# Kernel optimization log

Measured on AMD Instinct MI355X. Metric: run time of the kernel, lower is better.

## Reference

```python
import jax, jax.numpy as jnp
import numpy as np

B, S, HID = 2, 2048, 2048
NH, NKV, D = 16, 8, 128
EPS = 1e-6
THETA = 10000.0


def _rms_norm(x, w):
    # RMSNorm over last dim (head_dim), Qwen3-style per-head q/k norm
    var = jnp.mean(jnp.square(x), axis=-1, keepdims=True)
    return x * jax.lax.rsqrt(var + EPS) * w


def _rotate_half(x):
    x1, x2 = jnp.split(x, 2, axis=-1)
    return jnp.concatenate([-x2, x1], axis=-1)


def setup_inputs() -> dict:
    key = jax.random.key(0)
    ks = jax.random.split(key, 8)
    hidden_states = jax.random.normal(ks[0], (B, S, HID), dtype=jnp.float32)
    # rotary embeddings (HF-style: emb = concat(freqs, freqs))
    inv_freq = 1.0 / (THETA ** (jnp.arange(0, D, 2, dtype=jnp.float32) / D))
    pos = jnp.arange(S, dtype=jnp.float32)
    freqs = jnp.outer(pos, inv_freq)                      # [S, D/2]
    emb = jnp.concatenate([freqs, freqs], axis=-1)        # [S, D]
    cos = jnp.broadcast_to(jnp.cos(emb)[None], (B, S, D))
    sin = jnp.broadcast_to(jnp.sin(emb)[None], (B, S, D))
    w_scale = 1.0 / np.sqrt(HID)
    Wq = jax.random.normal(ks[1], (HID, NH * D), dtype=jnp.float32) * w_scale
    Wk = jax.random.normal(ks[2], (HID, NKV * D), dtype=jnp.float32) * w_scale
    Wv = jax.random.normal(ks[3], (HID, NKV * D), dtype=jnp.float32) * w_scale
    Wo = jax.random.normal(ks[4], (NH * D, HID), dtype=jnp.float32) * w_scale
    q_norm_w = jnp.ones((D,), dtype=jnp.float32)
    k_norm_w = jnp.ones((D,), dtype=jnp.float32)
    return {"hidden_states": hidden_states, "cos": cos, "sin": sin,
            "Wq": Wq, "Wk": Wk, "Wv": Wv, "Wo": Wo,
            "q_norm_w": q_norm_w, "k_norm_w": k_norm_w}


def reference(hidden_states, cos, sin, Wq, Wk, Wv, Wo, q_norm_w, k_norm_w):
    b, s, _ = hidden_states.shape
    # projections + per-head RMSNorm on q/k, then [B,H,S,D]
    q = _rms_norm((hidden_states @ Wq).reshape(b, s, NH, D), q_norm_w)
    k = _rms_norm((hidden_states @ Wk).reshape(b, s, NKV, D), k_norm_w)
    v = (hidden_states @ Wv).reshape(b, s, NKV, D)
    q = jnp.swapaxes(q, 1, 2)  # [B,NH,S,D]
    k = jnp.swapaxes(k, 1, 2)  # [B,NKV,S,D]
    v = jnp.swapaxes(v, 1, 2)
    # rotary position embedding
    c = cos[:, None, :, :]
    sn = sin[:, None, :, :]
    q = q * c + _rotate_half(q) * sn
    k = k * c + _rotate_half(k) * sn
    # GQA: expand kv heads to match query heads
    rep = NH // NKV
    k = jnp.repeat(k, rep, axis=1)
    v = jnp.repeat(v, rep, axis=1)
    # scaled causal attention (splash_attention semantics, causal mask)
    q = q * (D ** -0.5)
    scores = jnp.einsum('bhqd,bhkd->bhqk', q, k)
    causal = jnp.tril(jnp.ones((s, s), dtype=bool))
    scores = jnp.where(causal[None, None], scores, jnp.finfo(scores.dtype).min)
    attn = jax.nn.softmax(scores, axis=-1)
    out = jnp.einsum('bhqk,bhkd->bhqd', attn, v)
    out = jnp.swapaxes(out, 1, 2).reshape(b, s, NH * D)
    return out @ Wo
```

## Files before the change

### kernel.cpp

```cpp
#include <hip/hip_runtime.h>
#include <hip/hip_bf16.h>

typedef unsigned short u16;
typedef unsigned int u32;
typedef unsigned long long u64;
typedef __attribute__((ext_vector_type(8))) short short8;
typedef __attribute__((ext_vector_type(4))) float floatx4;

#define AS1 __attribute__((address_space(1)))
#define AS3 __attribute__((address_space(3)))

__device__ __forceinline__ float bf2f(u16 u) {
    u32 x = ((u32)u) << 16;
    float f;
    __builtin_memcpy(&f, &x, 4);
    return f;
}
__device__ __forceinline__ u16 f2bf(float f) {
    u32 x;
    __builtin_memcpy(&x, &f, 4);
    u32 r = (x + 0x7fffu + ((x >> 16) & 1u)) >> 16;
    return (u16)r;
}
__device__ __forceinline__ u32 f2bf_pk(float a, float b) {
    __hip_bfloat162 h = __float22bfloat162_rn(float2{a, b});
    u32 r;
    __builtin_memcpy(&r, &h, 4);
    return r;
}

__global__ __launch_bounds__(256) void convert_x(const float* __restrict__ in,
                                                 u16* __restrict__ out) {
    int i = blockIdx.x * 256 + threadIdx.x;
    float4 v = *(const float4*)(in + (size_t)i * 4);
    u16 o[4] = {f2bf(v.x), f2bf(v.y), f2bf(v.z), f2bf(v.w)};
    *(u64*)(out + (size_t)i * 4) = *(u64*)o;
}

__global__ __launch_bounds__(1024) void transpose_wall(const float* __restrict__ Wq,
                                                       const float* __restrict__ Wk,
                                                       const float* __restrict__ Wv,
                                                       const float* __restrict__ Wo,
                                                       u16* __restrict__ WqkvT,
                                                       u16* __restrict__ WoT) {
    const int z = blockIdx.z;
    const float* in;
    u16* out;
    int C;
    if (z == 0) { in = Wq; out = WqkvT; C = 2048; }
    else if (z == 1) { in = Wk; out = WqkvT + 2048 * 2048; C = 1024; }
    else if (z == 2) { in = Wv; out = WqkvT + 3072 * 2048; C = 1024; }
    else { in = Wo; out = WoT; C = 2048; }
    const int c0 = blockIdx.x * 32, r0 = blockIdx.y * 32;
    if (c0 >= C) return;
    __shared__ u16 t[32][33];
    const int tx = threadIdx.x, ty = threadIdx.y;
    t[ty][tx] = f2bf(in[(size_t)(r0 + ty) * C + c0 + tx]);
    __syncthreads();
    out[(size_t)(c0 + ty) * 2048 + r0 + tx] = t[tx][ty];
}

__global__ __launch_bounds__(1024) void transpose_v(const u16* __restrict__ QKV,
                                                    u16* __restrict__ Vt) {
    __shared__ u16 t[32][33];
    const int tx = threadIdx.x, ty = threadIdx.y;
    const int b = blockIdx.z >> 3, kv = blockIdx.z & 7;
    const int s0 = blockIdx.x * 32, d0 = blockIdx.y * 32;
    t[ty][tx] = QKV[(size_t)(b * 2048 + s0 + ty) * 4096 + 3072 + kv * 128 + d0 + tx];
    __syncthreads();
    Vt[(size_t)((b * 8 + kv) * 128 + d0 + ty) * 2048 + s0 + tx] = t[tx][ty];
}

template <typename OUT_T>
__global__ __launch_bounds__(256) void gemm_bt(const u16* __restrict__ A,
                                               const u16* __restrict__ Bt,
                                               OUT_T* __restrict__ C,
                                               int M, int N, int K) {
    __shared__ __align__(16) u16 As[128 * 64];
    __shared__ __align__(16) u16 Bs[128 * 64];
    const int tid = threadIdx.x;
    const int wave = tid >> 6, lane = tid & 63;
    const int lr = lane & 15, lq = lane >> 4;
    const int m0 = blockIdx.y * 128, n0 = blockIdx.x * 128;
    const int wr = (wave >> 1) * 64, wc = (wave & 1) * 64;

    floatx4 zf = {0.f, 0.f, 0.f, 0.f};
    floatx4 acc[4][4];
#pragma unroll
    for (int i = 0; i < 4; i++)
#pragma unroll
        for (int j = 0; j < 4; j++) acc[i][j] = zf;

    const int lrow = lane >> 3;
    const int lcol = (lane & 7) << 3;

    for (int k0 = 0; k0 < K; k0 += 64) {
        __syncthreads();
#pragma unroll
        for (int c = 0; c < 4; c++) {
            int chunk = (wave << 2) + c;
            int row = (chunk << 3) + lrow;
            __builtin_amdgcn_global_load_lds(
                (const AS1 void*)(A + (size_t)(m0 + row) * K + k0 + lcol),
                (AS3 void*)(As + (chunk << 9)), 16, 0, 0);
            __builtin_amdgcn_global_load_lds(
                (const AS1 void*)(Bt + (size_t)(n0 + row) * K + k0 + lcol),
                (AS3 void*)(Bs + (chunk << 9)), 16, 0, 0);
        }
        __syncthreads();
#pragma unroll
        for (int kk = 0; kk < 64; kk += 32) {
            short8 af[4], bfr[4];
#pragma unroll
            for (int i = 0; i < 4; i++)
                af[i] = *(const short8*)(As + (wr + i * 16 + lr) * 64 + kk + lq * 8);
#pragma unroll
            for (int j = 0; j < 4; j++)
                bfr[j] = *(const short8*)(Bs + (wc + j * 16 + lr) * 64 + kk + lq * 8);
#pragma unroll
            for (int i = 0; i < 4; i++)
#pragma unroll
                for (int j = 0; j < 4; j++)
                    acc[i][j] = __builtin_amdgcn_mfma_f32_16x16x32_bf16(af[i], bfr[j], acc[i][j], 0, 0, 0);
        }
    }
#pragma unroll
    for (int i = 0; i < 4; i++)
#pragma unroll
        for (int j = 0; j < 4; j++)
#pragma unroll
            for (int r = 0; r < 4; r++) {
                int row = m0 + wr + i * 16 + lq * 4 + r;
                int col = n0 + wc + j * 16 + lr;
                if constexpr (sizeof(OUT_T) == 2)
                    C[(size_t)row * N + col] = f2bf(acc[i][j][r]);
                else
                    C[(size_t)row * N + col] = acc[i][j][r];
            }
}

__global__ __launch_bounds__(256) void norm_rope(u16* __restrict__ QKV,
                                                 const float* __restrict__ cosb,
                                                 const float* __restrict__ sinb,
                                                 const float* __restrict__ qw,
                                                 const float* __restrict__ kw) {
    const int tid = threadIdx.x;
    const int wave = tid >> 6, lane = tid & 63;
    const int t = blockIdx.x * 4 + wave;
    u16* ptr;
    const float* w;
    float scale;
    int bs;
    if (t < 65536) {
        bs = t >> 4;
        ptr = QKV + (size_t)bs * 4096 + (t & 15) * 128;
        w = qw;
        scale = 0.08838834764831845f * 1.4426950408889634f;
    } else {
        int t2 = t - 65536;
        bs = t2 >> 3;
        ptr = QKV + (size_t)bs * 4096 + 2048 + (t2 & 7) * 128;
        w = kw;
        scale = 1.0f;
    }
    const int d = lane * 2;
    u32 xv = *(const u32*)(ptr + d);
    float x0 = bf2f((u16)(xv & 0xffff)), x1 = bf2f((u16)(xv >> 16));
    float ss = x0 * x0 + x1 * x1;
#pragma unroll
    for (int off = 1; off < 64; off <<= 1) ss += __shfl_xor(ss, off);
    float rn = rsqrtf(ss * (1.0f / 128.0f) + 1e-6f);
    float2 wv = *(const float2*)(w + d);
    float y0 = x0 * rn * wv.x;
    float y1 = x1 * rn * wv.y;
    float p0 = __shfl_xor(y0, 32);
    float p1 = __shfl_xor(y1, 32);
    float sgn = (lane < 32) ? -1.0f : 1.0f;
    float2 cv = *(const float2*)(cosb + (size_t)bs * 128 + d);
    float2 sv = *(const float2*)(sinb + (size_t)bs * 128 + d);
    float o0 = (y0 * cv.x + sgn * p0 * sv.x) * scale;
    float o1 = (y1 * cv.y + sgn * p1 * sv.y) * scale;
    *(u32*)(ptr + d) = (u32)f2bf(o0) | ((u32)f2bf(o1) << 16);
}

__global__ __launch_bounds__(512, 2) void attn_kernel(const u16* __restrict__ QKV,
                                                      const u16* __restrict__ Vt,
                                                      u16* __restrict__ O) {
    __shared__ __align__(16) u16 Ks[2][64 * 128];
    __shared__ __align__(16) u16 Vs[2][128 * 64];
    const int tid = threadIdx.x;
    const int wave = tid >> 6, lane = tid & 63;
    const int lr = lane & 15, lq = lane >> 4;
    const int h = blockIdx.y, b = blockIdx.z;
    const int qt = (b == 0) ? (15 - blockIdx.x) : blockIdx.x;
    const int kv = h >> 1;
    const int q0 = qt * 128;
    const int wq = wave * 16;

    auto stage = [&](int buf, int k0s) {
#pragma unroll
        for (int j = 0; j < 2; j++) {
            int r = wave * 8 + j * 4 + (lane >> 4);
            int c = (lane & 15) ^ (r & 15);
            __builtin_amdgcn_global_load_lds(
                (const AS1 void*)(QKV + (size_t)(b * 2048 + k0s + r) * 4096 + 2048 + kv * 128 + c * 8),
                (AS3 void*)(&Ks[buf][(wave * 8 + j * 4) * 128]), 16, 0, 0);
        }
#pragma unroll
        for (int j = 0; j < 2; j++) {
            int r = wave * 16 + j * 8 + (lane >> 3);
            int c = (lane & 7) ^ (r & 7);
            __builtin_amdgcn_global_load_lds(
                (const AS1 void*)(Vt + (size_t)((b * 8 + kv) * 128 + r) * 2048 + k0s + c * 8),
                (AS3 void*)(&Vs[buf][(wave * 16 + j * 8) * 64]), 16, 0, 0);
        }
    };

    short8 qf[4];
#pragma unroll
    for (int t = 0; t < 4; t++)
        qf[t] = *(const short8*)(QKV + (size_t)(b * 2048 + q0 + wq + lr) * 4096 + h * 128 + t * 32 + lq * 8);

    floatx4 zf = {0.f, 0.f, 0.f, 0.f};
    floatx4 oacc[8];
#pragma unroll
    for (int jn = 0; jn < 8; jn++) oacc[jn] = zf;
    float mstate = -1e30f;
    float lstate = 0.f;

    const int nIter = (qt + 1) * 2;

    stage(0, 0);

    for (int kt = 0; kt < nIter; kt++) {
        const int k0 = kt * 64;
        const int cur = kt & 1;
        __syncthreads();
        if (kt + 1 < nIter) stage(cur ^ 1, k0 + 64);

        if (k0 <= q0 + wq + 15) {
            const u16* KsC = &Ks[cur][0];
            const u16* VsC = &Vs[cur][0];
            floatx4 sacc[4];
#pragma unroll
            for (int jm = 0; jm < 4; jm++) sacc[jm] = zf;
#pragma unroll
            for (int t = 0; t < 4; t++) {
                short8 a[4];
#pragma unroll
                for (int jm = 0; jm < 4; jm++)
                    a[jm] = *(const short8*)(KsC + (jm * 16 + lr) * 128 + (((t * 4 + lq) ^ lr) << 3));
#pragma unroll
                for (int jm = 0; jm < 4; jm++)
                    sacc[jm] = __builtin_amdgcn_mfma_f32_16x16x32_bf16(a[jm], qf[t], sacc[jm], 0, 0, 0);
            }

            if (k0 + 63 > q0 + wq) {
#pragma unroll
                for (int jm = 0; jm < 4; jm++) {
                    int diff = (q0 + wq + lr) - (k0 + jm * 16 + lq * 4);
#pragma unroll
                    for (int r = 0; r < 4; r++)
                        if (r > diff) sacc[jm][r] = -1e30f;
                }
            }

            float mx = -1e30f;
#pragma unroll
            for (int jm = 0; jm < 4; jm++)
#pragma unroll
                for (int r = 0; r < 4; r++) mx = fmaxf(mx, sacc[jm][r]);
            mx = fmaxf(mx, __shfl_xor(mx, 16));
            mx = fmaxf(mx, __shfl_xor(mx, 32));
            float mnew = fmaxf(mstate, mx);
            float alpha = exp2f(mstate - mnew);
            mstate = mnew;
            float rs = 0.f;
#pragma unroll
            for (int jm = 0; jm < 4; jm++)
#pragma unroll
                for (int r = 0; r < 4; r++) {
                    float p = exp2f(sacc[jm][r] - mnew);
                    sacc[jm][r] = p;
                    rs += p;
                }
            rs += __shfl_xor(rs, 16);
            rs += __shfl_xor(rs, 32);
            lstate = lstate * alpha + rs;

            u64 pb[4];
#pragma unroll
            for (int jm = 0; jm < 4; jm++) {
                u32 lo = f2bf_pk(sacc[jm][0], sacc[jm][1]);
                u32 hi = f2bf_pk(sacc[jm][2], sacc[jm][3]);
                pb[jm] = (u64)lo | ((u64)hi << 32);
            }

            float ao[4];
#pragma unroll
            for (int r = 0; r < 4; r++) ao[r] = __shfl(alpha, lq * 4 + r);
#pragma unroll
            for (int jn = 0; jn < 8; jn++)
#pragma unroll
                for (int r = 0; r < 4; r++) oacc[jn][r] *= ao[r];

#pragma unroll
            for (int t = 0; t < 2; t++) {
                union { short8 v; u64 q[2]; } pa;
                pa.q[0] = pb[2 * t];
                pa.q[1] = pb[2 * t + 1];
#pragma unroll
                for (int jn = 0; jn < 8; jn++) {
                    const u16* vrow = VsC + (jn * 16 + lr) * 64 + (lq & 1) * 4;
                    union { short8 v; u64 q[2]; } vb;
                    vb.q[0] = *(const u64*)(vrow + (((t * 4 + (lq >> 1)) ^ (lr & 7)) << 3));
                    vb.q[1] = *(const u64*)(vrow + (((t * 4 + 2 + (lq >> 1)) ^ (lr & 7)) << 3));
                    oacc[jn] = __builtin_amdgcn_mfma_f32_16x16x32_bf16(pa.v, vb.v, oacc[jn], 0, 0, 0);
                }
            }
        }
    }

    float lo[4];
#pragma unroll
    for (int r = 0; r < 4; r++) lo[r] = __shfl(lstate, lq * 4 + r);
#pragma unroll
    for (int jn = 0; jn < 8; jn++)
#pragma unroll
        for (int r = 0; r < 4; r++) {
            int row = q0 + wq + lq * 4 + r;
            O[(size_t)(b * 2048 + row) * 2048 + h * 128 + jn * 16 + lr] =
                f2bf(oacc[jn][r] / lo[r]);
        }
}

extern "C" void kernel_launch(void* const* d_in, const int* in_sizes, int n_in,
                              void* d_out, int out_size, void* d_ws, size_t ws_size,
                              hipStream_t stream) {
    const float* X = (const float*)d_in[0];
    const float* cosb = (const float*)d_in[1];
    const float* sinb = (const float*)d_in[2];
    const float* Wq = (const float*)d_in[3];
    const float* Wk = (const float*)d_in[4];
    const float* Wv = (const float*)d_in[5];
    const float* Wo = (const float*)d_in[6];
    const float* qw = (const float*)d_in[7];
    const float* kw = (const float*)d_in[8];
    float* out = (float*)d_out;
    u16* ws = (u16*)d_ws;

    u16* WqkvT = ws;
    u16* WoT = WqkvT + 8388608;
    u16* Xb = WoT + 4194304;
    u16* QKVb = Xb + 8388608;
    u16* Vtb = QKVb + 16777216;
    u16* Ob = Xb;

    dim3 tb(32, 32);
    transpose_wall<<<dim3(64, 64, 4), tb, 0, stream>>>(Wq, Wk, Wv, Wo, WqkvT, WoT);
    convert_x<<<8192, 256, 0, stream>>>(X, Xb);

    gemm_bt<u16><<<dim3(32, 32), 256, 0, stream>>>(Xb, WqkvT, QKVb, 4096, 4096, 2048);

    norm_rope<<<24576, 256, 0, stream>>>(QKVb, cosb, sinb, qw, kw);
    transpose_v<<<dim3(64, 4, 16), tb, 0, stream>>>(QKVb, Vtb);

    attn_kernel<<<dim3(16, 16, 2), 512, 0, stream>>>(QKVb, Vtb, Ob);

    gemm_bt<float><<<dim3(16, 32), 256, 0, stream>>>(Ob, WoT, out, 4096, 2048, 2048);
}
```

Measured before the change: 407.1 us.

## Replace GEMM with 256x256 double-buffered, swizzled LDS pipelined kernel

Replaces the 128x128 single-buffered GEMM with a 256x256 tile kernel using 8 waves, double-buffered LDS, XOR-swizzled layout to avoid bank conflicts, and interleaved async global-to-LDS loads between MFMA phases with explicit waitcnt/barriers and setprio. It targets exposed memory latency and low data reuse in both projection GEMMs. The larger tiles mean fewer blocks (256 and 128), which may underfill the 256 CUs, and the hand-tuned vmcnt counting is fragile.

```diff
diff --git a/kernel.cpp b/kernel.cpp
--- a/kernel.cpp
+++ b/kernel.cpp
@@ -72,70 +72,148 @@
 }
 
 template <typename OUT_T>
-__global__ __launch_bounds__(256) void gemm_bt(const u16* __restrict__ A,
-                                               const u16* __restrict__ Bt,
-                                               OUT_T* __restrict__ C,
-                                               int M, int N, int K) {
-    __shared__ __align__(16) u16 As[128 * 64];
-    __shared__ __align__(16) u16 Bs[128 * 64];
+__global__ __launch_bounds__(512, 2) void gemm256(const u16* __restrict__ A,
+                                                  const u16* __restrict__ Bt,
+                                                  OUT_T* __restrict__ C,
+                                                  int M, int N, int K) {
+    (void)M;
+    __shared__ __align__(16) u16 lds[2][2][2][128 * 64];
     const int tid = threadIdx.x;
     const int wave = tid >> 6, lane = tid & 63;
     const int lr = lane & 15, lq = lane >> 4;
-    const int m0 = blockIdx.y * 128, n0 = blockIdx.x * 128;
-    const int wr = (wave >> 1) * 64, wc = (wave & 1) * 64;
+    const int wm = wave >> 2, wn = wave & 3;
+    const int m0 = blockIdx.y * 256, n0 = blockIdx.x * 256;
+
+    const int srow = lane >> 3;
+    const int schunk = ((lane & 7) ^ srow) << 3;
+    const int slot = wave << 1;
+
+    auto stage = [&](const u16* src, int rbase, int buf, int mat, int half, int k0) {
+#pragma unroll
+        for (int j = 0; j < 2; j++) {
+            int r = rbase + half * 128 + (slot + j) * 8 + srow;
+            __builtin_amdgcn_global_load_lds(
+                (const AS1 void*)(src + (size_t)r * K + k0 + schunk),
+                (AS3 void*)(&lds[buf][mat][half][(slot + j) * 512]), 16, 0, 0);
+        }
+    };
 
     floatx4 zf = {0.f, 0.f, 0.f, 0.f};
-    floatx4 acc[4][4];
-#pragma unroll
-    for (int i = 0; i < 4; i++)
-#pragma unroll
-        for (int j = 0; j < 4; j++) acc[i][j] = zf;
-
-    const int lrow = lane >> 3;
-    const int lcol = (lane & 7) << 3;
-
-    for (int k0 = 0; k0 < K; k0 += 64) {
-        __syncthreads();
-#pragma unroll
-        for (int c = 0; c < 4; c++) {
-            int chunk = (wave << 2) + c;
-            int row = (chunk << 3) + lrow;
-            __builtin_amdgcn_global_load_lds(
-                (const AS1 void*)(A + (size_t)(m0 + row) * K + k0 + lcol),
-                (AS3 void*)(As + (chunk << 9)), 16, 0, 0);
-            __builtin_amdgcn_global_load_lds(
-                (const AS1 void*)(Bt + (size_t)(n0 + row) * K + k0 + lcol),
-                (AS3 void*)(Bs + (chunk << 9)), 16, 0, 0);
-        }
-        __syncthreads();
-#pragma unroll
-        for (int kk = 0; kk < 64; kk += 32) {
-            short8 af[4], bfr[4];
-#pragma unroll
-            for (int i = 0; i < 4; i++)
-                af[i] = *(const short8*)(As + (wr + i * 16 + lr) * 64 + kk + lq * 8);
-#pragma unroll
-            for (int j = 0; j < 4; j++)
-                bfr[j] = *(const short8*)(Bs + (wc + j * 16 + lr) * 64 + kk + lq * 8);
-#pragma unroll
-            for (int i = 0; i < 4; i++)
-#pragma unroll
-                for (int j = 0; j < 4; j++)
-                    acc[i][j] = __builtin_amdgcn_mfma_f32_16x16x32_bf16(af[i], bfr[j], acc[i][j], 0, 0, 0);
-        }
+    floatx4 acc[8][4];
+#pragma unroll
+    for (int i = 0; i < 8; i++)
+#pragma unroll
+        for (int jn = 0; jn < 4; jn++) acc[i][jn] = zf;
+
+    const int NT = K >> 6;
+
+    stage(Bt, n0, 0, 1, 0, 0);
+    stage(Bt, n0, 0, 1, 1, 0);
+    stage(A, m0, 0, 0, 0, 0);
+    stage(A, m0, 0, 0, 1, 0);
+    if (NT > 1) {
+        stage(Bt, n0, 1, 1, 0, 64);
+        stage(Bt, n0, 1, 1, 1, 64);
+        stage(A, m0, 1, 0, 0, 64);
+        asm volatile("s_waitcnt vmcnt(6)" ::: "memory");
+    } else {
+        asm volatile("s_waitcnt vmcnt(0)" ::: "memory");
     }
-#pragma unroll
-    for (int i = 0; i < 4; i++)
-#pragma unroll
-        for (int j = 0; j < 4; j++)
+    __builtin_amdgcn_s_barrier();
+
+    for (int kt = 0; kt < NT; kt++) {
+        const int b = kt & 1;
+        const u16* Ab = &lds[b][0][wm][0];
+        const u16* Bb = &lds[b][1][wn >> 1][0];
+        const int brow = (wn & 1) * 64;
+        const int sx = lr & 7;
+        const int nk = (kt + 2) << 6;
+
+        short8 bf0[4], bf1[4], af[4];
+#pragma unroll
+        for (int jn = 0; jn < 4; jn++) {
+            int rh = brow + jn * 16 + lr;
+            bf0[jn] = *(const short8*)(Bb + rh * 64 + ((lq ^ sx) << 3));
+            bf1[jn] = *(const short8*)(Bb + rh * 64 + (((4 + lq) ^ sx) << 3));
+        }
+#pragma unroll
+        for (int i = 0; i < 4; i++)
+            af[i] = *(const short8*)(Ab + (i * 16 + lr) * 64 + ((lq ^ sx) << 3));
+        if (kt + 1 < NT) stage(A, m0, b ^ 1, 0, 1, (kt + 1) << 6);
+        __builtin_amdgcn_s_barrier();
+        asm volatile("s_waitcnt lgkmcnt(0)" ::: "memory");
+        __builtin_amdgcn_sched_barrier(0);
+        __builtin_amdgcn_s_setprio(1);
+#pragma unroll
+        for (int i = 0; i < 4; i++)
+#pragma unroll
+            for (int jn = 0; jn < 4; jn++)
+                acc[i][jn] = __builtin_amdgcn_mfma_f32_16x16x32_bf16(af[i], bf0[jn], acc[i][jn], 0, 0, 0);
+        __builtin_amdgcn_s_setprio(0);
+        __builtin_amdgcn_s_barrier();
+
+        short8 ag[4];
+#pragma unroll
+        for (int i = 0; i < 4; i++)
+            ag[i] = *(const short8*)(Ab + ((i + 4) * 16 + lr) * 64 + ((lq ^ sx) << 3));
+        if (kt + 2 < NT) stage(Bt, n0, b, 1, 0, nk);
+        __builtin_amdgcn_s_barrier();
+        asm volatile("s_waitcnt lgkmcnt(0)" ::: "memory");
+        __builtin_amdgcn_sched_barrier(0);
+        __builtin_amdgcn_s_setprio(1);
+#pragma unroll
+        for (int i = 0; i < 4; i++)
+#pragma unroll
+            for (int jn = 0; jn < 4; jn++)
+                acc[i + 4][jn] = __builtin_amdgcn_mfma_f32_16x16x32_bf16(ag[i], bf0[jn], acc[i + 4][jn], 0, 0, 0);
+        __builtin_amdgcn_s_setprio(0);
+        __builtin_amdgcn_s_barrier();
+
+        short8 c0[4], c1[4];
+#pragma unroll
+        for (int i = 0; i < 4; i++) {
+            c0[i] = *(const short8*)(Ab + (i * 16 + lr) * 64 + (((4 + lq) ^ sx) << 3));
+            c1[i] = *(const short8*)(Ab + ((i + 4) * 16 + lr) * 64 + (((4 + lq) ^ sx) << 3));
+        }
+        if (kt + 2 < NT) stage(Bt, n0, b, 1, 1, nk);
+        __builtin_amdgcn_s_barrier();
+        asm volatile("s_waitcnt lgkmcnt(0)" ::: "memory");
+        __builtin_amdgcn_sched_barrier(0);
+        __builtin_amdgcn_s_setprio(1);
+#pragma unroll
+        for (int i = 0; i < 4; i++)
+#pragma unroll
+            for (int jn = 0; jn < 4; jn++)
+                acc[i][jn] = __builtin_amdgcn_mfma_f32_16x16x32_bf16(c0[i], bf1[jn], acc[i][jn], 0, 0, 0);
+        __builtin_amdgcn_s_setprio(0);
+        __builtin_amdgcn_s_barrier();
+
+        if (kt + 2 < NT) stage(A, m0, b, 0, 0, nk);
+        __builtin_amdgcn_s_barrier();
+        __builtin_amdgcn_s_setprio(1);
+#pragma unroll
+        for (int i = 0; i < 4; i++)
+#pragma unroll
+            for (int jn = 0; jn < 4; jn++)
+                acc[i + 4][jn] = __builtin_amdgcn_mfma_f32_16x16x32_bf16(c1[i], bf1[jn], acc[i + 4][jn], 0, 0, 0);
+        __builtin_amdgcn_s_setprio(0);
+        if (kt + 2 < NT) asm volatile("s_waitcnt vmcnt(6)" ::: "memory");
+        else asm volatile("s_waitcnt vmcnt(0)" ::: "memory");
+        __builtin_amdgcn_s_barrier();
+    }
+
+#pragma unroll
+    for (int i = 0; i < 8; i++)
+#pragma unroll
+        for (int jn = 0; jn < 4; jn++)
 #pragma unroll
             for (int r = 0; r < 4; r++) {
-                int row = m0 + wr + i * 16 + lq * 4 + r;
-                int col = n0 + wc + j * 16 + lr;
+                int row = m0 + wm * 128 + i * 16 + lq * 4 + r;
+                int col = n0 + wn * 64 + jn * 16 + lr;
                 if constexpr (sizeof(OUT_T) == 2)
-                    C[(size_t)row * N + col] = f2bf(acc[i][j][r]);
+                    C[(size_t)row * N + col] = f2bf(acc[i][jn][r]);
                 else
-                    C[(size_t)row * N + col] = acc[i][j][r];
+                    C[(size_t)row * N + col] = acc[i][jn][r];
             }
 }
 
@@ -360,12 +438,12 @@
     transpose_wall<<<dim3(64, 64, 4), tb, 0, stream>>>(Wq, Wk, Wv, Wo, WqkvT, WoT);
     convert_x<<<8192, 256, 0, stream>>>(X, Xb);
 
-    gemm_bt<u16><<<dim3(32, 32), 256, 0, stream>>>(Xb, WqkvT, QKVb, 4096, 4096, 2048);
+    gemm256<u16><<<dim3(16, 16), 512, 0, stream>>>(Xb, WqkvT, QKVb, 4096, 4096, 2048);
 
     norm_rope<<<24576, 256, 0, stream>>>(QKVb, cosb, sinb, qw, kw);
     transpose_v<<<dim3(64, 4, 16), tb, 0, stream>>>(QKVb, Vtb);
 
     attn_kernel<<<dim3(16, 16, 2), 512, 0, stream>>>(QKVb, Vtb, Ob);
 
-    gemm_bt<float><<<dim3(16, 32), 256, 0, stream>>>(Ob, WoT, out, 4096, 2048, 2048);
-}
+    gemm256<float><<<dim3(8, 16), 512, 0, stream>>>(Ob, WoT, out, 4096, 2048, 2048);
+}
```

Result: faster. 384.4 us (-5.6%).
